# Kernel tuning notes

Measured on AMD Instinct MI355X. Metric: run time of the kernel, lower is better.

Reference implementation:

```python
import jax, jax.numpy as jnp
import numpy as np

NUM_CLASSES = 21
EPS = 1e-6


def setup_inputs() -> dict:
    key = jax.random.key(0)
    k1, k2, k3 = jax.random.split(key, 3)
    feats = jax.random.normal(k1, (8, 256, 64, 64), dtype=jnp.float32)
    preds = jax.random.normal(k2, (8, NUM_CLASSES, 256, 256), dtype=jnp.float32)
    # labels in [0, 22): includes nclass=21 which acts as an ignore label
    masks = jax.random.randint(k3, (8, 256, 256), 0, 22, dtype=jnp.int64)
    return {"feats": feats, "preds": preds, "masks": masks}


def reference(feats, preds, masks):
    B, C = feats.shape[0], feats.shape[1]
    H, W = masks.shape[-2:]
    K = NUM_CLASSES

    # argmax over class logits -> predicted label map [B, H, W]
    pred_lbl = jnp.argmax(preds, axis=1)

    # bilinear upsample (align_corners=False, matches half-pixel resize)
    feats_up = jax.image.resize(feats, (B, C, H, W), method="bilinear")

    cls = jnp.arange(K)
    # one-hot of gt mask and of predictions; labels >= K (incl. 255) fall in
    # the dropped last channel of one_hot_2d, i.e. match no class here.
    gt_oh = (masks[:, None, :, :] == cls[None, :, None, None])      # [B,K,H,W]
    pr_oh = (pred_lbl[:, None, :, :] == cls[None, :, None, None])   # [B,K,H,W]
    joint = (gt_oh & pr_oh).astype(feats_up.dtype)                  # [B,K,H,W]

    counts = joint.sum(axis=(2, 3))                                  # [B,K]
    sums = jnp.einsum("bchw,bkhw->bkc", feats_up, joint)            # [B,K,C]

    # per-image class means (absent classes -> 0/eps = 0), then batch mean
    proto = (sums / (counts[..., None] + EPS)).mean(axis=0)          # [K,C]
    return proto
```

## Files before the change

### kernel.cpp

```cpp
#include <hip/hip_runtime.h>

#define KC   21
#define BB   8
#define CC   256
#define HWP  65536
#define SRC  4096
#define NS   128
#define PC   32
#define FST  257

#define WSF_PARTW 32768
#define WSF_PART  (WSF_PARTW + BB*NS*KC)

__global__ __launch_bounds__(256, 2)
void k1_classify(const float* __restrict__ preds,
                 const int*   __restrict__ masks,
                 unsigned char* __restrict__ L,
                 float* __restrict__ out)
{
    int tid = threadIdx.x;
    if (blockIdx.x == 0) {
        float4* o4 = reinterpret_cast<float4*>(out);
#pragma unroll
        for (int i = 0; i < (KC * CC / 4 + 255) / 256; ++i) {
            int j = tid + i * 256;
            if (j < KC * CC / 4) o4[j] = make_float4(0.f, 0.f, 0.f, 0.f);
        }
    }

    int idx = blockIdx.x * 256 + tid;
    int b   = idx >> 14;
    int hw4 = (idx & 16383) << 2;

    const float* pb = preds + (size_t)b * KC * HWP + hw4;
    float va[4][KC];
#pragma unroll
    for (int k = 0; k < KC; ++k) {
        float4 t = *reinterpret_cast<const float4*>(pb + (size_t)k * HWP);
        va[0][k] = t.x; va[1][k] = t.y; va[2][k] = t.z; va[3][k] = t.w;
    }

    int4 mm = *reinterpret_cast<const int4*>(masks + b * HWP + hw4);
    int mk[4] = { mm.x, mm.y, mm.z, mm.w };

    uchar4 r;
    unsigned char* rp = reinterpret_cast<unsigned char*>(&r);
#pragma unroll
    for (int j = 0; j < 4; ++j) {
        float best = va[j][0];
        int   bi   = 0;
#pragma unroll
        for (int k = 1; k < KC; ++k) {
            if (va[j][k] > best) { best = va[j][k]; bi = k; }
        }
        rp[j] = (mk[j] == bi) ? (unsigned char)bi : (unsigned char)255;
    }
    *reinterpret_cast<uchar4*>(L + (size_t)b * HWP + hw4) = r;
}

__global__ __launch_bounds__(128)
void k2_contract(const float* __restrict__ feats,
                 const unsigned char* __restrict__ L,
                 float* __restrict__ partial,
                 float* __restrict__ partialw)
{
    __shared__ float fs[PC * FST];
    __shared__ float ws[KC * PC];
    int s = blockIdx.x, b = blockIdx.y;
    int tid = threadIdx.x;
    int y = s >> 1, x0c = (s & 1) * PC;
    int p0 = y * 64 + x0c;

    for (int t = tid; t < KC * PC / 4; t += 128)
        *reinterpret_cast<float4*>(ws + t * 4) = make_float4(0.f, 0.f, 0.f, 0.f);
    __syncthreads();

    {
        int q = tid & 7, c0 = tid >> 3;
#pragma unroll
        for (int i = 0; i < 16; ++i) {
            int c = i * 16 + c0;
            float4 f4 = *reinterpret_cast<const float4*>(
                feats + (size_t)(b * CC + c) * SRC + p0 + q * 4);
            fs[(q * 4 + 0) * FST + c] = f4.x;
            fs[(q * 4 + 1) * FST + c] = f4.y;
            fs[(q * 4 + 2) * FST + c] = f4.z;
            fs[(q * 4 + 3) * FST + c] = f4.w;
        }
    }

    {
        int r = tid >> 4, cb = tid & 15;
        int h = 4 * y - 2 + r;
        if ((unsigned)h < 256u) {
            float sy = h * 0.25f - 0.375f;
            int   yt = (int)floorf(sy);
            float wy = sy - (float)yt;
            int ya = yt < 0 ? 0 : yt;
            int yb = yt + 1 > 63 ? 63 : yt + 1;
            float wyy = ((ya == y) ? (1.f - wy) : 0.f) + ((yb == y) ? wy : 0.f);
            if (wyy != 0.f) {
                const unsigned char* Lrow = L + ((size_t)b << 16) + ((size_t)h << 8);
                int wb0 = 4 * x0c - 2;
#pragma unroll
                for (int j = 0; j < 9; ++j) {
                    int col = cb + j * 16;
                    int w = wb0 + col;
                    if (col < 136 && (unsigned)w < 256u) {
                        int k = Lrow[w];
                        if (k < KC) {
                            float sx = w * 0.25f - 0.375f;
                            int   xt = (int)floorf(sx);
                            float wx = sx - (float)xt;
                            int xa = xt < 0 ? 0 : xt;
                            int xb = xt + 1 > 63 ? 63 : xt + 1;
                            if (xa >= x0c && xa < x0c + PC)
                                atomicAdd(&ws[k * PC + xa - x0c], wyy * (1.f - wx));
                            if (xb >= x0c && xb < x0c + PC)
                                atomicAdd(&ws[k * PC + xb - x0c], wyy * wx);
                        }
                    }
                }
            }
        }
    }
    __syncthreads();

    float f0[PC], f1[PC];
#pragma unroll
    for (int p = 0; p < PC; ++p) {
        f0[p] = fs[p * FST + tid];
        f1[p] = fs[p * FST + tid + 128];
    }

    float* op = partial + ((size_t)(b * NS + s)) * KC * CC + tid;
#pragma unroll 3
    for (int k = 0; k < KC; ++k) {
        const float* wk = ws + k * PC;
        float a00 = 0.f, a01 = 0.f, a02 = 0.f, a03 = 0.f;
        float a10 = 0.f, a11 = 0.f, a12 = 0.f, a13 = 0.f;
#pragma unroll
        for (int q = 0; q < PC / 4; ++q) {
            float4 w4 = *reinterpret_cast<const float4*>(wk + q * 4);
            a00 += w4.x * f0[q * 4 + 0];
            a01 += w4.y * f0[q * 4 + 1];
            a02 += w4.z * f0[q * 4 + 2];
            a03 += w4.w * f0[q * 4 + 3];
            a10 += w4.x * f1[q * 4 + 0];
            a11 += w4.y * f1[q * 4 + 1];
            a12 += w4.z * f1[q * 4 + 2];
            a13 += w4.w * f1[q * 4 + 3];
        }
        op[(size_t)k * CC]       = (a00 + a01) + (a02 + a03);
        op[(size_t)k * CC + 128] = (a10 + a11) + (a12 + a13);
    }

    if (tid < KC) {
        float sw = 0.f;
#pragma unroll
        for (int p = 0; p < PC; ++p) sw += ws[tid * PC + ((p + tid) & (PC - 1))];
        partialw[(size_t)(b * NS + s) * KC + tid] = sw;
    }
}

__global__ __launch_bounds__(256)
void k3_finalize(const float* __restrict__ partial,
                 const float* __restrict__ partialw,
                 float* __restrict__ out)
{
    int k = blockIdx.x, b = blockIdx.y;
    int tid = threadIdx.x;

    const float* base = partial + ((size_t)(b * NS) * KC + k) * CC + tid;
    float acc = 0.f;
#pragma unroll 8
    for (int s = 0; s < NS; ++s) acc += base[(size_t)s * KC * CC];

    __shared__ float red[2];
    float v = 0.f;
    if (tid < NS) v = partialw[(size_t)(b * NS + tid) * KC + k];
#pragma unroll
    for (int off = 32; off; off >>= 1) v += __shfl_down(v, off);
    if (tid < NS && (tid & 63) == 0) red[tid >> 6] = v;
    __syncthreads();
    float cnt = red[0] + red[1];

    atomicAdd(&out[k * CC + tid], acc / (8.f * (cnt + 1e-6f)));
}

extern "C" void kernel_launch(void* const* d_in, const int* in_sizes, int n_in,
                              void* d_out, int out_size, void* d_ws, size_t ws_size,
                              hipStream_t stream) {
    const float* feats = (const float*)d_in[0];
    const float* preds = (const float*)d_in[1];
    const int*   masks = (const int*)  d_in[2];
    float* out = (float*)d_out;

    float* wsf = (float*)d_ws;
    unsigned char* L = (unsigned char*)d_ws;
    float* partialw = wsf + WSF_PARTW;
    float* partial  = wsf + WSF_PART;

    k1_classify<<<(BB * HWP / 4) / 256, 256, 0, stream>>>(preds, masks, L, out);
    k2_contract<<<dim3(NS, BB), 128, 0, stream>>>(feats, L, partial, partialw);
    k3_finalize<<<dim3(KC, BB), 256, 0, stream>>>(partial, partialw, out);
}
```

Before: 38.83 us.

## Double k2 block size and split pixel reduction across two thread halves

The contraction kernel now runs 256 threads per block instead of 128. Each half of the block takes 16 of the 32 source pixels for all 256 channels, and the two halves' per-class partial sums are combined through shared memory before the store. The feature load and label scatter loops are re-strided to fit the larger block. This aims to raise per-CU parallelism and cut per-thread register and instruction load, at the cost of an extra barrier and a shared-memory reduction pass.

```diff
diff --git a/kernel.cpp b/kernel.cpp
--- a/kernel.cpp
+++ b/kernel.cpp
@@ -58,7 +58,7 @@
     *reinterpret_cast<uchar4*>(L + (size_t)b * HWP + hw4) = r;
 }
 
-__global__ __launch_bounds__(128)
+__global__ __launch_bounds__(256, 4)
 void k2_contract(const float* __restrict__ feats,
                  const unsigned char* __restrict__ L,
                  float* __restrict__ partial,
@@ -71,15 +71,15 @@
     int y = s >> 1, x0c = (s & 1) * PC;
     int p0 = y * 64 + x0c;
 
-    for (int t = tid; t < KC * PC / 4; t += 128)
-        *reinterpret_cast<float4*>(ws + t * 4) = make_float4(0.f, 0.f, 0.f, 0.f);
+    if (tid < KC * PC / 4)
+        *reinterpret_cast<float4*>(ws + tid * 4) = make_float4(0.f, 0.f, 0.f, 0.f);
     __syncthreads();
 
     {
         int q = tid & 7, c0 = tid >> 3;
 #pragma unroll
-        for (int i = 0; i < 16; ++i) {
-            int c = i * 16 + c0;
+        for (int i = 0; i < 8; ++i) {
+            int c = i * 32 + c0;
             float4 f4 = *reinterpret_cast<const float4*>(
                 feats + (size_t)(b * CC + c) * SRC + p0 + q * 4);
             fs[(q * 4 + 0) * FST + c] = f4.x;
@@ -90,7 +90,7 @@
     }
 
     {
-        int r = tid >> 4, cb = tid & 15;
+        int r = tid >> 5, cb = tid & 31;
         int h = 4 * y - 2 + r;
         if ((unsigned)h < 256u) {
             float sy = h * 0.25f - 0.375f;
@@ -103,8 +103,8 @@
                 const unsigned char* Lrow = L + ((size_t)b << 16) + ((size_t)h << 8);
                 int wb0 = 4 * x0c - 2;
 #pragma unroll
-                for (int j = 0; j < 9; ++j) {
-                    int col = cb + j * 16;
+                for (int j = 0; j < 5; ++j) {
+                    int col = cb + j * 32;
                     int w = wb0 + col;
                     if (col < 136 && (unsigned)w < 256u) {
                         int k = Lrow[w];
@@ -126,21 +126,32 @@
     }
     __syncthreads();
 
-    float f0[PC], f1[PC];
-#pragma unroll
-    for (int p = 0; p < PC; ++p) {
-        f0[p] = fs[p * FST + tid];
-        f1[p] = fs[p * FST + tid + 128];
-    }
-
-    float* op = partial + ((size_t)(b * NS + s)) * KC * CC + tid;
-#pragma unroll 3
+    int cp   = tid & 127;
+    int psub = tid >> 7;
+    int pw   = psub * 16;
+
+    float f0[16], f1[16];
+#pragma unroll
+    for (int p = 0; p < 16; ++p) {
+        f0[p] = fs[(pw + p) * FST + cp];
+        f1[p] = fs[(pw + p) * FST + cp + 128];
+    }
+
+    float swcnt = 0.f;
+    if (tid < KC) {
+#pragma unroll
+        for (int p = 0; p < PC; ++p) swcnt += ws[tid * PC + ((p + tid) & (PC - 1))];
+    }
+    __syncthreads();
+
+    float acc0[KC], acc1[KC];
+#pragma unroll
     for (int k = 0; k < KC; ++k) {
-        const float* wk = ws + k * PC;
+        const float* wk = ws + k * PC + pw;
         float a00 = 0.f, a01 = 0.f, a02 = 0.f, a03 = 0.f;
         float a10 = 0.f, a11 = 0.f, a12 = 0.f, a13 = 0.f;
 #pragma unroll
-        for (int q = 0; q < PC / 4; ++q) {
+        for (int q = 0; q < 4; ++q) {
             float4 w4 = *reinterpret_cast<const float4*>(wk + q * 4);
             a00 += w4.x * f0[q * 4 + 0];
             a01 += w4.y * f0[q * 4 + 1];
@@ -151,16 +162,30 @@
             a12 += w4.z * f1[q * 4 + 2];
             a13 += w4.w * f1[q * 4 + 3];
         }
-        op[(size_t)k * CC]       = (a00 + a01) + (a02 + a03);
-        op[(size_t)k * CC + 128] = (a10 + a11) + (a12 + a13);
-    }
-
-    if (tid < KC) {
-        float sw = 0.f;
-#pragma unroll
-        for (int p = 0; p < PC; ++p) sw += ws[tid * PC + ((p + tid) & (PC - 1))];
-        partialw[(size_t)(b * NS + s) * KC + tid] = sw;
-    }
+        acc0[k] = (a00 + a01) + (a02 + a03);
+        acc1[k] = (a10 + a11) + (a12 + a13);
+    }
+
+    float* scr = fs;
+    if (psub == 1) {
+#pragma unroll
+        for (int k = 0; k < KC; ++k) {
+            scr[k * 256 + cp]       = acc0[k];
+            scr[k * 256 + 128 + cp] = acc1[k];
+        }
+    }
+    __syncthreads();
+    if (psub == 0) {
+        float* op = partial + ((size_t)(b * NS + s)) * KC * CC + cp;
+#pragma unroll
+        for (int k = 0; k < KC; ++k) {
+            op[(size_t)k * CC]       = acc0[k] + scr[k * 256 + cp];
+            op[(size_t)k * CC + 128] = acc1[k] + scr[k * 256 + 128 + cp];
+        }
+    }
+
+    if (tid < KC)
+        partialw[(size_t)(b * NS + s) * KC + tid] = swcnt;
 }
 
 __global__ __launch_bounds__(256)
@@ -202,6 +227,6 @@
     float* partial  = wsf + WSF_PART;
 
     k1_classify<<<(BB * HWP / 4) / 256, 256, 0, stream>>>(preds, masks, L, out);
-    k2_contract<<<dim3(NS, BB), 128, 0, stream>>>(feats, L, partial, partialw);
+    k2_contract<<<dim3(NS, BB), 256, 0, stream>>>(feats, L, partial, partialw);
     k3_finalize<<<dim3(KC, BB), 256, 0, stream>>>(partial, partialw, out);
 }
```

Result: faster. 37.14 us (-4.3%).
